# Performance work log

Measured on AMD Instinct MI355X. Metric: run time of the kernel, lower is better.

## Reference

```python
import jax, jax.numpy as jnp
import numpy as np

D = 128  # hidden_size

def setup_inputs() -> dict:
    key = jax.random.key(0)
    ks = jax.random.split(key, 10)
    N, K = 50000, 32
    x = jax.random.normal(ks[0], (N, D), dtype=jnp.float32)
    x_nb = jax.random.normal(ks[1], (N, K, D), dtype=jnp.float32)
    weight = jax.random.uniform(ks[2], (N, K), dtype=jnp.float32)
    s = 1.0 / np.sqrt(D)
    Wx = jax.random.uniform(ks[3], (D, D), jnp.float32, -s, s)
    bx = jax.random.uniform(ks[4], (D,), jnp.float32, -s, s)
    Wn = jax.random.uniform(ks[5], (D, D), jnp.float32, -s, s)
    bn = jax.random.uniform(ks[6], (D,), jnp.float32, -s, s)
    Ww = jax.random.uniform(ks[7], (D, 1), jnp.float32, -1.0, 1.0)
    bw = jax.random.uniform(ks[8], (D,), jnp.float32, -1.0, 1.0)
    Wl = jax.random.uniform(ks[9], (1, D), jnp.float32, -s, s)
    bl = jnp.zeros((1,), jnp.float32)
    return {"x": x, "x_nb": x_nb, "weight": weight,
            "Wx": Wx, "bx": bx, "Wn": Wn, "bn": bn,
            "Ww": Ww, "bw": bw, "Wl": Wl, "bl": bl}

def reference(x, x_nb, weight, Wx, bx, Wn, bn, Ww, bw, Wl, bl):
    # x: [N, d], x_nb: [N, K, d], weight: [N, K]
    x_s = x @ Wx.T + bx                      # [N, d]
    n_s = jnp.einsum('nkd,ed->nke', x_nb, Wn) + bn   # [N, K, d]
    w = weight[..., None] * Ww[:, 0] + bw    # [N, K, d] (Linear(1,d))
    h = x_s[:, None, :] + n_s + w            # [N, K, d]
    h = jnp.where(h >= 0, h, 0.1 * h)        # LeakyReLU(0.1)
    scores = jnp.einsum('nkd,d->nk', h, Wl[0]) + bl[0]  # [N, K]
    attn = jax.nn.softmax(scores, axis=1)    # softmax over neighbors
    out = jnp.einsum('nk,nkd->nd', attn, x_nb)
    return out
```

## Files before the change

kernel.cpp:

```cpp
#include <hip/hip_runtime.h>

#define D 128
#define KN 32

typedef __bf16 bf16x8 __attribute__((ext_vector_type(8)));
typedef float f32x4 __attribute__((ext_vector_type(4)));

__device__ __forceinline__ unsigned bfpack2(float a, float b) {
  unsigned ua = __float_as_uint(a), ub = __float_as_uint(b);
  ua += 0x7FFFu + ((ua >> 16) & 1u);
  ub += 0x7FFFu + ((ub >> 16) & 1u);
  return (ua >> 16) | (ub & 0xFFFF0000u);
}
__device__ __forceinline__ uint4 pack8(const float4& a, const float4& b) {
  uint4 r;
  r.x = bfpack2(a.x, a.y); r.y = bfpack2(a.z, a.w);
  r.z = bfpack2(b.x, b.y); r.w = bfpack2(b.z, b.w);
  return r;
}

__device__ __forceinline__ void lgkm_barrier() {
  __builtin_amdgcn_sched_barrier(0);
  asm volatile("s_waitcnt lgkmcnt(0)" ::: "memory");
  __builtin_amdgcn_s_barrier();
  __builtin_amdgcn_sched_barrier(0);
}


__device__ __forceinline__ void stage128_512(const float* __restrict__ src, int nrows,
                                             uint4* buf, int tid) {
  float4 v[4][2];
  #pragma unroll
  for (int i = 0; i < 4; ++i) {
    const int c = i * 512 + tid;
    const int row = c >> 4, slot = c & 15;
    if (row < nrows) {
      const float4* p = (const float4*)(src + (size_t)row * D + slot * 8);
      v[i][0] = p[0]; v[i][1] = p[1];
    } else {
      v[i][0] = make_float4(0.f, 0.f, 0.f, 0.f);
      v[i][1] = make_float4(0.f, 0.f, 0.f, 0.f);
    }
  }
  #pragma unroll
  for (int i = 0; i < 4; ++i) {
    const int c = i * 512 + tid;
    const int row = c >> 4, slot = c & 15;
    buf[row * 16 + (slot ^ (row & 7))] = pack8(v[i][0], v[i][1]);
  }
}

__device__ __forceinline__ void stage128_256(const float* __restrict__ src,
                                             uint4* buf, int tid) {
  #pragma unroll
  for (int i = 0; i < 8; ++i) {
    const int c = i * 256 + tid;
    const int row = c >> 4, slot = c & 15;
    const float4* p = (const float4*)(src + (size_t)row * D + slot * 8);
    buf[row * 16 + (slot ^ (row & 7))] = pack8(p[0], p[1]);
  }
}

__device__ __forceinline__ void stage64_load(const float* __restrict__ src, int tid,
                                             float4 v[4][2]) {
  #pragma unroll
  for (int i = 0; i < 4; ++i) {
    const int c = i * 256 + tid;
    const int row = c >> 4, slot = c & 15;
    const float4* p = (const float4*)(src + (size_t)row * D + slot * 8);
    v[i][0] = p[0]; v[i][1] = p[1];
  }
}
__device__ __forceinline__ void stage64_write(uint4* buf, int tid,
                                              const float4 v[4][2]) {
  #pragma unroll
  for (int i = 0; i < 4; ++i) {
    const int c = i * 256 + tid;
    const int row = c >> 4, slot = c & 15;
    buf[row * 16 + (slot ^ (row & 7))] = pack8(v[i][0], v[i][1]);
  }
}

__global__ __launch_bounds__(512, 4) void base_mfma(
    const float* __restrict__ x, const float* __restrict__ Wx,
    const float* __restrict__ bx, const float* __restrict__ bn,
    const float* __restrict__ bw, float* __restrict__ out, int N)
{
  __shared__ uint4 Bb[2048];
  __shared__ uint4 Ab[2048];
  __shared__ float bvec[D];
  const int tid = threadIdx.x;

  stage128_512(Wx, 128, Bb, tid);
  if (tid < D) bvec[tid] = bx[tid] + bn[tid] + bw[tid];

  const int lane = tid & 63, li = lane & 15, g = lane >> 4;
  const int wv = tid >> 6, rq = wv >> 1, ch = wv & 1;
  const int ntiles = (N + 127) >> 7;

  for (int t = blockIdx.x; t < ntiles; t += gridDim.x) {
    const int r0t = t << 7;
    __syncthreads();
    stage128_512(x + (size_t)r0t * D, N - r0t, Ab, tid);
    __syncthreads();

    f32x4 acc[2][4];
    #pragma unroll
    for (int i = 0; i < 2; ++i)
      #pragma unroll
      for (int j = 0; j < 4; ++j) acc[i][j] = (f32x4){0.f, 0.f, 0.f, 0.f};

    #pragma unroll
    for (int kb = 0; kb < 4; ++kb) {
      const int slot = kb * 4 + g;
      const int r0 = rq * 32 + li, r1 = r0 + 16;
      const bf16x8 a0 = __builtin_bit_cast(bf16x8, Ab[r0 * 16 + (slot ^ (r0 & 7))]);
      const bf16x8 a1 = __builtin_bit_cast(bf16x8, Ab[r1 * 16 + (slot ^ (r1 & 7))]);
      #pragma unroll
      for (int ct = 0; ct < 4; ++ct) {
        const int e = ch * 64 + ct * 16 + li;
        const bf16x8 b = __builtin_bit_cast(bf16x8, Bb[e * 16 + (slot ^ (e & 7))]);
        acc[0][ct] = __builtin_amdgcn_mfma_f32_16x16x32_bf16(a0, b, acc[0][ct], 0, 0, 0);
        acc[1][ct] = __builtin_amdgcn_mfma_f32_16x16x32_bf16(a1, b, acc[1][ct], 0, 0, 0);
      }
    }

    #pragma unroll
    for (int rt = 0; rt < 2; ++rt) {
      #pragma unroll
      for (int reg = 0; reg < 4; ++reg) {
        const int r = r0t + rq * 32 + rt * 16 + 4 * g + reg;
        if (r < N) {
          #pragma unroll
          for (int ct = 0; ct < 4; ++ct) {
            const int e = ch * 64 + ct * 16 + li;
            out[(size_t)r * D + e] = acc[rt][ct][reg] + bvec[e];
          }
        }
      }
    }
  }
}

__global__ __launch_bounds__(256, 3) void gnn_mfma(
    const float* __restrict__ x_nb, const float* __restrict__ weight,
    const float* __restrict__ Wn, const float* __restrict__ Ww,
    const float* __restrict__ Wl, float* __restrict__ out, int N)
{
  __shared__ uint4 Bb[2048];
  __shared__ uint4 Ab[1024];
  __shared__ float basel[2 * D];
  __shared__ float wwl[D], wll[D];
  __shared__ float wgt[2 * KN];
  __shared__ float spart[2][2][KN];
  __shared__ float attnl[2 * KN];
  const int tid = threadIdx.x;

  stage128_256(Wn, Bb, tid);
  if (tid < D) { wwl[tid] = Ww[tid]; wll[tid] = Wl[tid]; }

  const int lane = tid & 63, li = lane & 15, g = lane >> 4;
  const int wv = tid >> 6, rq = wv >> 1, ch = wv & 1;
  const int ntiles = N >> 1;

  float4 v[4][2];
  float basev = 0.f, wgtv = 0.f;

  int t = blockIdx.x;
  {
    stage64_load(x_nb + (size_t)(2 * t) * KN * D, tid, v);
    basev = out[(size_t)(2 * t) * D + tid];
    if (tid < 2 * KN) wgtv = weight[(size_t)(2 * t) * KN + tid];
    stage64_write(Ab, tid, v);
    basel[tid] = basev;
    if (tid < 2 * KN) wgt[tid] = wgtv;
  }
  __syncthreads();

  for (; t < ntiles; t += gridDim.x) {
    const int tn = t + gridDim.x;
    const bool have_next = (tn < ntiles);
    if (have_next) {
      stage64_load(x_nb + (size_t)(2 * tn) * KN * D, tid, v);
      basev = out[(size_t)(2 * tn) * D + tid];
      if (tid < 2 * KN) wgtv = weight[(size_t)(2 * tn) * KN + tid];
    }

    f32x4 acc[2][4];
    #pragma unroll
    for (int i = 0; i < 2; ++i)
      #pragma unroll
      for (int j = 0; j < 4; ++j) acc[i][j] = (f32x4){0.f, 0.f, 0.f, 0.f};

    #pragma unroll
    for (int kb = 0; kb < 4; ++kb) {
      const int slot = kb * 4 + g;
      const int r0 = rq * 32 + li, r1 = r0 + 16;
      const bf16x8 a0 = __builtin_bit_cast(bf16x8, Ab[r0 * 16 + (slot ^ (r0 & 7))]);
      const bf16x8 a1 = __builtin_bit_cast(bf16x8, Ab[r1 * 16 + (slot ^ (r1 & 7))]);
      #pragma unroll
      for (int ct = 0; ct < 4; ++ct) {
        const int e = ch * 64 + ct * 16 + li;
        const bf16x8 b = __builtin_bit_cast(bf16x8, Bb[e * 16 + (slot ^ (e & 7))]);
        acc[0][ct] = __builtin_amdgcn_mfma_f32_16x16x32_bf16(a0, b, acc[0][ct], 0, 0, 0);
        acc[1][ct] = __builtin_amdgcn_mfma_f32_16x16x32_bf16(a1, b, acc[1][ct], 0, 0, 0);
      }
    }

    float bvv[4], wwv[4], wlv[4];
    #pragma unroll
    for (int ct = 0; ct < 4; ++ct) {
      const int e = ch * 64 + ct * 16 + li;
      bvv[ct] = basel[rq * D + e];
      wwv[ct] = wwl[e];
      wlv[ct] = wll[e];
    }
    #pragma unroll
    for (int rt = 0; rt < 2; ++rt) {
      #pragma unroll
      for (int reg = 0; reg < 4; ++reg) {
        const int k = rt * 16 + 4 * g + reg;
        const float wk = wgt[rq * KN + k];
        float p = 0.f;
        #pragma unroll
        for (int ct = 0; ct < 4; ++ct) {
          float h = acc[rt][ct][reg] + bvv[ct] + wk * wwv[ct];
          h = fmaxf(h, 0.1f * h);
          p = fmaf(h, wlv[ct], p);
        }
        p += __shfl_xor(p, 1);
        p += __shfl_xor(p, 2);
        p += __shfl_xor(p, 4);
        p += __shfl_xor(p, 8);
        if (li == 0) spart[ch][rq][k] = p;
      }
    }
    lgkm_barrier();

    if (tid < 64) {
      const int node = tid >> 5, k = tid & 31;
      const float s = spart[0][node][k] + spart[1][node][k];
      float mx = s;
      #pragma unroll
      for (int m = 16; m >= 1; m >>= 1) mx = fmaxf(mx, __shfl_xor(mx, m));
      const float pe = __expf(s - mx);
      float sum = pe;
      #pragma unroll
      for (int m = 16; m >= 1; m >>= 1) sum += __shfl_xor(sum, m);
      attnl[node * KN + k] = pe / sum;
    }
    lgkm_barrier();

    if (wv < 2) {
      const int node = wv;
      const int slot = lane & 15, kg = lane >> 4;
      float p8[8];
      #pragma unroll
      for (int j = 0; j < 8; ++j) p8[j] = 0.f;
      #pragma unroll
      for (int kk = 0; kk < 8; ++kk) {
        const int k = kg * 8 + kk;
        const int row = node * KN + k;
        const uint4 u = Ab[row * 16 + (slot ^ kk)];
        const float a = attnl[node * KN + k];
        const unsigned uw[4] = {u.x, u.y, u.z, u.w};
        #pragma unroll
        for (int q = 0; q < 4; ++q) {
          p8[2 * q]     = fmaf(a, __uint_as_float(uw[q] << 16), p8[2 * q]);
          p8[2 * q + 1] = fmaf(a, __uint_as_float(uw[q] & 0xFFFF0000u), p8[2 * q + 1]);
        }
      }
      #pragma unroll
      for (int j = 0; j < 8; ++j) p8[j] += __shfl_xor(p8[j], 16);
      #pragma unroll
      for (int j = 0; j < 8; ++j) p8[j] += __shfl_xor(p8[j], 32);
      if (kg == 0) {
        float* o = out + (size_t)(2 * t + node) * D + slot * 8;
        *(float4*)(o)     = make_float4(p8[0], p8[1], p8[2], p8[3]);
        *(float4*)(o + 4) = make_float4(p8[4], p8[5], p8[6], p8[7]);
      }
    }
    lgkm_barrier();

    if (have_next) {
      stage64_write(Ab, tid, v);
      basel[tid] = basev;
      if (tid < 2 * KN) wgt[tid] = wgtv;
    }
    lgkm_barrier();
  }
}

extern "C" void kernel_launch(void* const* d_in, const int* in_sizes, int n_in,
                              void* d_out, int out_size, void* d_ws, size_t ws_size,
                              hipStream_t stream) {
  const float* x      = (const float*)d_in[0];
  const float* x_nb   = (const float*)d_in[1];
  const float* weight = (const float*)d_in[2];
  const float* Wx     = (const float*)d_in[3];
  const float* bx     = (const float*)d_in[4];
  const float* Wn     = (const float*)d_in[5];
  const float* bn     = (const float*)d_in[6];
  const float* Ww     = (const float*)d_in[7];
  const float* bw     = (const float*)d_in[8];
  const float* Wl     = (const float*)d_in[9];
  float* out = (float*)d_out;
  const int N = in_sizes[0] / D;

  base_mfma<<<dim3(391), dim3(512), 0, stream>>>(x, Wx, bx, bn, bw, out, N);
  gnn_mfma<<<dim3(768), dim3(256), 0, stream>>>(x_nb, weight, Wn, Ww, Wl, out, N);
}
```

Measured before the change: 201.7 us.

## Compute softmax redundantly per wave and spread aggregation over all four waves

Every wave now computes the per-node softmax itself from the score partials and broadcasts the attention weights with shuffles. This removes the attn shared buffer and one block barrier. The weighted neighbor aggregation is split across all four waves, each handling half the feature columns of one node, where previously only two waves did it. The bf16 packing also switches from a manual bit-twiddling round to compiler casts, which may map to hardware convert instructions. The cost is redundant softmax work and an extra shuffle-reduction stage.

```diff
diff --git a/kernel.cpp b/kernel.cpp
--- a/kernel.cpp
+++ b/kernel.cpp
@@ -6,17 +6,11 @@
 typedef __bf16 bf16x8 __attribute__((ext_vector_type(8)));
 typedef float f32x4 __attribute__((ext_vector_type(4)));
 
-__device__ __forceinline__ unsigned bfpack2(float a, float b) {
-  unsigned ua = __float_as_uint(a), ub = __float_as_uint(b);
-  ua += 0x7FFFu + ((ua >> 16) & 1u);
-  ub += 0x7FFFu + ((ub >> 16) & 1u);
-  return (ua >> 16) | (ub & 0xFFFF0000u);
-}
 __device__ __forceinline__ uint4 pack8(const float4& a, const float4& b) {
-  uint4 r;
-  r.x = bfpack2(a.x, a.y); r.y = bfpack2(a.z, a.w);
-  r.z = bfpack2(b.x, b.y); r.w = bfpack2(b.z, b.w);
-  return r;
+  bf16x8 v8;
+  v8[0] = (__bf16)a.x; v8[1] = (__bf16)a.y; v8[2] = (__bf16)a.z; v8[3] = (__bf16)a.w;
+  v8[4] = (__bf16)b.x; v8[5] = (__bf16)b.y; v8[6] = (__bf16)b.z; v8[7] = (__bf16)b.w;
+  return __builtin_bit_cast(uint4, v8);
 }
 
 __device__ __forceinline__ void lgkm_barrier() {
@@ -153,7 +147,6 @@
   __shared__ float wwl[D], wll[D];
   __shared__ float wgt[2 * KN];
   __shared__ float spart[2][2][KN];
-  __shared__ float attnl[2 * KN];
   const int tid = threadIdx.x;
 
   stage128_256(Wn, Bb, tid);
@@ -162,6 +155,7 @@
   const int lane = tid & 63, li = lane & 15, g = lane >> 4;
   const int wv = tid >> 6, rq = wv >> 1, ch = wv & 1;
   const int ntiles = N >> 1;
+  const int gr = gridDim.x;
 
   float4 v[4][2];
   float basev = 0.f, wgtv = 0.f;
@@ -177,8 +171,8 @@
   }
   __syncthreads();
 
-  for (; t < ntiles; t += gridDim.x) {
-    const int tn = t + gridDim.x;
+  for (; t < ntiles; t += gr) {
+    const int tn = t + gr;
     const bool have_next = (tn < ntiles);
     if (have_next) {
       stage64_load(x_nb + (size_t)(2 * tn) * KN * D, tid, v);
@@ -237,9 +231,10 @@
     }
     lgkm_barrier();
 
-    if (tid < 64) {
-      const int node = tid >> 5, k = tid & 31;
-      const float s = spart[0][node][k] + spart[1][node][k];
+    float attn;
+    {
+      const int ks = lane & 31;
+      const float s = spart[0][rq][ks] + spart[1][rq][ks];
       float mx = s;
       #pragma unroll
       for (int m = 16; m >= 1; m >>= 1) mx = fmaxf(mx, __shfl_xor(mx, m));
@@ -247,35 +242,37 @@
       float sum = pe;
       #pragma unroll
       for (int m = 16; m >= 1; m >>= 1) sum += __shfl_xor(sum, m);
-      attnl[node * KN + k] = pe / sum;
-    }
-    lgkm_barrier();
-
-    if (wv < 2) {
-      const int node = wv;
-      const int slot = lane & 15, kg = lane >> 4;
+      attn = pe / sum;
+    }
+
+    {
+      const int slot8 = lane & 7, kg = lane >> 3;
+      float ak[4];
+      #pragma unroll
+      for (int kk = 0; kk < 4; ++kk) ak[kk] = __shfl(attn, kg * 4 + kk);
       float p8[8];
       #pragma unroll
       for (int j = 0; j < 8; ++j) p8[j] = 0.f;
       #pragma unroll
-      for (int kk = 0; kk < 8; ++kk) {
-        const int k = kg * 8 + kk;
-        const int row = node * KN + k;
-        const uint4 u = Ab[row * 16 + (slot ^ kk)];
-        const float a = attnl[node * KN + k];
+      for (int kk = 0; kk < 4; ++kk) {
+        const int k = kg * 4 + kk;
+        const int row = rq * KN + k;
+        const uint4 u = Ab[row * 16 + ((ch * 8 + slot8) ^ (row & 7))];
         const unsigned uw[4] = {u.x, u.y, u.z, u.w};
         #pragma unroll
         for (int q = 0; q < 4; ++q) {
-          p8[2 * q]     = fmaf(a, __uint_as_float(uw[q] << 16), p8[2 * q]);
-          p8[2 * q + 1] = fmaf(a, __uint_as_float(uw[q] & 0xFFFF0000u), p8[2 * q + 1]);
+          p8[2 * q]     = fmaf(ak[kk], __uint_as_float(uw[q] << 16), p8[2 * q]);
+          p8[2 * q + 1] = fmaf(ak[kk], __uint_as_float(uw[q] & 0xFFFF0000u), p8[2 * q + 1]);
         }
       }
       #pragma unroll
-      for (int j = 0; j < 8; ++j) p8[j] += __shfl_xor(p8[j], 16);
-      #pragma unroll
-      for (int j = 0; j < 8; ++j) p8[j] += __shfl_xor(p8[j], 32);
+      for (int j = 0; j < 8; ++j) {
+        p8[j] += __shfl_xor(p8[j], 8);
+        p8[j] += __shfl_xor(p8[j], 16);
+        p8[j] += __shfl_xor(p8[j], 32);
+      }
       if (kg == 0) {
-        float* o = out + (size_t)(2 * t + node) * D + slot * 8;
+        float* o = out + (size_t)(2 * t + rq) * D + ch * 64 + slot8 * 8;
         *(float4*)(o)     = make_float4(p8[0], p8[1], p8[2], p8[3]);
         *(float4*)(o + 4) = make_float4(p8[4], p8[5], p8[6], p8[7]);
       }
```

Measured after the change: 220.4 us. 9.3% more time.
